# Kernel optimization log

Measured on AMD Instinct MI355X. Metric: run time of the kernel, lower is better.

## Reference

```python
import jax, jax.numpy as jnp
from jax import lax
import numpy as np

N, C, H, W = 8, 256, 96, 96
K = 5            # d_conv=4 forced odd -> 5 in FauxScan1D
HID = 2 * C      # ff_mult * dim


def setup_inputs() -> dict:
    key = jax.random.key(0)
    ks = iter(jax.random.split(key, 40))
    nrm = lambda *s: jax.random.normal(next(ks), s, jnp.float32) * 0.02
    inp = {'x': jax.random.normal(next(ks), (N, C, H, W), jnp.float32)}
    inp['ln1_w'] = jnp.ones((C,), jnp.float32)
    inp['ln1_b'] = jnp.zeros((C,), jnp.float32)
    inp['dw_w'] = nrm(3, 3, 1, C)   # depthwise 3x3, HWIO with feature_group_count=C
    inp['dw_b'] = jnp.zeros((C,), jnp.float32)
    for d in ('lr', 'rl', 'tb', 'bt'):
        inp[d + '_dw_w'] = nrm(K, 1, C)   # depthwise conv1d, WIO
        inp[d + '_dw_b'] = jnp.zeros((C,), jnp.float32)
        inp[d + '_g_w'] = nrm(C, C)       # 1x1 gate conv (out, in)
        inp[d + '_g_b'] = jnp.zeros((C,), jnp.float32)
    inp['fuse_w'] = nrm(C, C)
    inp['fuse_b'] = jnp.zeros((C,), jnp.float32)
    inp['ln2_w'] = jnp.ones((C,), jnp.float32)
    inp['ln2_b'] = jnp.zeros((C,), jnp.float32)
    inp['ff1_w'] = nrm(2 * HID, C)
    inp['ff1_b'] = jnp.zeros((2 * HID,), jnp.float32)
    inp['ff2_w'] = nrm(C, HID)
    inp['ff2_b'] = jnp.zeros((C,), jnp.float32)
    return inp


def _ln2d(x, w, b, eps=1e-6):
    # LayerNorm2d: per-(sample, channel) stats over H,W
    m = x.mean(axis=(2, 3), keepdims=True)
    v = ((x - m) ** 2).mean(axis=(2, 3), keepdims=True)
    return (x - m) * lax.rsqrt(v + eps) * w[None, :, None, None] + b[None, :, None, None]


def _scan1d(seq, dw_w, dw_b, g_w, g_b):
    # FauxScan1D: seq (B, L, C) -> dwconv1d(k=5, pad=2) * sigmoid(pointwise gate)
    c = seq.shape[-1]
    y = lax.conv_general_dilated(seq, dw_w, (1,), [(K // 2, K // 2)],
                                 dimension_numbers=('NWC', 'WIO', 'NWC'),
                                 feature_group_count=c) + dw_b
    g = jax.nn.sigmoid(jnp.einsum('blc,dc->bld', seq, g_w) + g_b)
    return y * g


def _forward(x, ln1_w, ln1_b, dw_w, dw_b,
             lr_dw_w, lr_dw_b, lr_g_w, lr_g_b,
             rl_dw_w, rl_dw_b, rl_g_w, rl_g_b,
             tb_dw_w, tb_dw_b, tb_g_w, tb_g_b,
             bt_dw_w, bt_dw_b, bt_g_w, bt_g_b,
             fuse_w, fuse_b, ln2_w, ln2_b, ff1_w, ff1_b, ff2_w, ff2_b):
    n, c, hh, ww = x.shape
    y = _ln2d(x, ln1_w, ln1_b)
    y = lax.conv_general_dilated(y, dw_w, (1, 1), [(1, 1), (1, 1)],
                                 dimension_numbers=('NCHW', 'HWIO', 'NCHW'),
                                 feature_group_count=c) + dw_b[None, :, None, None]
    y = jnp.transpose(y, (0, 2, 3, 1))  # NHWC
    # lr: rows as sequences
    o = _scan1d(y.reshape(n * hh, ww, c), lr_dw_w, lr_dw_b, lr_g_w, lr_g_b).reshape(n, hh, ww, c)
    # rl: flip width, scan, flip back
    yf = jnp.flip(y, 2).reshape(n * hh, ww, c)
    o = o + jnp.flip(_scan1d(yf, rl_dw_w, rl_dw_b, rl_g_w, rl_g_b).reshape(n, hh, ww, c), 2)
    # tb: columns as sequences
    yt = jnp.transpose(y, (0, 2, 1, 3)).reshape(n * ww, hh, c)
    o = o + jnp.transpose(_scan1d(yt, tb_dw_w, tb_dw_b, tb_g_w, tb_g_b).reshape(n, ww, hh, c), (0, 2, 1, 3))
    # bt: flip height, columns, scan, undo
    yb = jnp.transpose(jnp.flip(y, 1), (0, 2, 1, 3)).reshape(n * ww, hh, c)
    o = o + jnp.flip(jnp.transpose(_scan1d(yb, bt_dw_w, bt_dw_b, bt_g_w, bt_g_b).reshape(n, ww, hh, c), (0, 2, 1, 3)), 1)
    y = jnp.transpose(o, (0, 3, 1, 2))  # back to NCHW
    y = jnp.einsum('nchw,dc->ndhw', y, fuse_w) + fuse_b[None, :, None, None]
    x = x + y
    z = _ln2d(x, ln2_w, ln2_b)
    z = jnp.einsum('nchw,dc->ndhw', z, ff1_w) + ff1_b[None, :, None, None]
    a, g = jnp.split(z, 2, axis=1)  # GLU on channel dim
    z = a * jax.nn.sigmoid(g)
    z = jnp.einsum('nchw,dc->ndhw', z, ff2_w) + ff2_b[None, :, None, None]
    return x + z


def reference(x, ln1_w, ln1_b, dw_w, dw_b,
              lr_dw_w, lr_dw_b, lr_g_w, lr_g_b,
              rl_dw_w, rl_dw_b, rl_g_w, rl_g_b,
              tb_dw_w, tb_dw_b, tb_g_w, tb_g_b,
              bt_dw_w, bt_dw_b, bt_g_w, bt_g_b,
              fuse_w, fuse_b, ln2_w, ln2_b, ff1_w, ff1_b, ff2_w, ff2_b):
    return _forward(x, ln1_w, ln1_b, dw_w, dw_b,
                    lr_dw_w, lr_dw_b, lr_g_w, lr_g_b,
                    rl_dw_w, rl_dw_b, rl_g_w, rl_g_b,
                    tb_dw_w, tb_dw_b, tb_g_w, tb_g_b,
                    bt_dw_w, bt_dw_b, bt_g_w, bt_g_b,
                    fuse_w, fuse_b, ln2_w, ln2_b, ff1_w, ff1_b, ff2_w, ff2_b)
```

## Files before the change

kernel.cpp:

```cpp
#include <hip/hip_runtime.h>

#define TPB 256
#define HWSZ 9216

typedef __attribute__((ext_vector_type(8))) short short8x;
typedef __attribute__((ext_vector_type(4))) float f32x4;
typedef unsigned short ushort_t;
typedef unsigned int uint_t;

__device__ __forceinline__ float sigf(float v) { return 1.0f / (1.0f + __expf(-v)); }

__device__ __forceinline__ ushort_t f2bf(float f) {
  __bf16 h = (__bf16)f;
  return __builtin_bit_cast(ushort_t, h);
}
__device__ __forceinline__ float bf2f(ushort_t h) {
  return __uint_as_float(((uint_t)h) << 16);
}

__global__ __launch_bounds__(TPB) void k_pack(
    const float* __restrict__ lrg, const float* __restrict__ rlg,
    const float* __restrict__ tbg, const float* __restrict__ btg,
    const float* __restrict__ fusew, const float* __restrict__ ff1w,
    const float* __restrict__ ff2w,
    ushort_t* __restrict__ Gp, ushort_t* __restrict__ Ftp,
    ushort_t* __restrict__ W1p, ushort_t* __restrict__ W2p) {
  int i = blockIdx.x * TPB + threadIdx.x;
  if (i < 262144) {
    int d = i >> 16, r = i & 65535;
    int kt = r >> 13, nt = (r >> 9) & 15, l = (r >> 3) & 63, j = r & 7;
    int k = kt * 32 + (l >> 4) * 8 + j;
    int n_ = nt * 16 + (l & 15);
    const float* g = (d == 0) ? lrg : (d == 1) ? rlg : (d == 2) ? tbg : btg;
    Gp[i] = f2bf(g[n_ * 256 + k]);
  } else if (i < 327680) {
    int r = i - 262144;
    int kt = r >> 13, nt = (r >> 9) & 15, l = (r >> 3) & 63, j = r & 7;
    int k = kt * 32 + (l >> 4) * 8 + j;
    int n_ = nt * 16 + (l & 15);
    Ftp[r] = f2bf(fusew[n_ * 256 + k]);
  } else if (i < 589824) {
    int r = i - 327680;
    int kt = r >> 15, pb = (r >> 10) & 31, ag = (r >> 9) & 1;
    int l = (r >> 3) & 63, j = r & 7;
    int k = kt * 32 + (l >> 4) * 8 + j;
    int colb = pb * 16 + (l & 15);
    int col = ag ? (512 + colb) : colb;
    W1p[r] = f2bf(ff1w[col * 256 + k]);
  } else if (i < 720896) {
    int r = i - 589824;
    int kt = r >> 13, nt = (r >> 9) & 15, l = (r >> 3) & 63, j = r & 7;
    int k = kt * 32 + (l >> 4) * 8 + j;
    int n_ = nt * 16 + (l & 15);
    W2p[r] = f2bf(ff2w[n_ * 512 + k]);
  }
}

__global__ __launch_bounds__(TPB) void k_stats(const float* __restrict__ src,
                                               float* __restrict__ mean,
                                               float* __restrict__ rstd) {
  int nc = blockIdx.x;
  const float4* p = (const float4*)(src + (long)nc * HWSZ);
  float s = 0.f, s2 = 0.f;
  for (int i = threadIdx.x; i < 2304; i += TPB) {
    float4 v = p[i];
    s += (v.x + v.y) + (v.z + v.w);
    s2 = fmaf(v.x, v.x, fmaf(v.y, v.y, fmaf(v.z, v.z, fmaf(v.w, v.w, s2))));
  }
#pragma unroll
  for (int off = 32; off > 0; off >>= 1) {
    s += __shfl_down(s, off);
    s2 += __shfl_down(s2, off);
  }
  __shared__ float ls[4], ls2[4];
  int lane = threadIdx.x & 63, wv = threadIdx.x >> 6;
  if (lane == 0) { ls[wv] = s; ls2[wv] = s2; }
  __syncthreads();
  if (threadIdx.x == 0) {
    float S = ls[0] + ls[1] + ls[2] + ls[3];
    float S2 = ls2[0] + ls2[1] + ls2[2] + ls2[3];
    float m = S * (1.0f / HWSZ);
    float var = S2 * (1.0f / HWSZ) - m * m;
    mean[nc] = m;
    rstd[nc] = rsqrtf(fmaxf(var, 0.f) + 1e-6f);
  }
}

__global__ __launch_bounds__(TPB) void k_lndw(
    const float* __restrict__ x, const float* __restrict__ mean1,
    const float* __restrict__ rstd1, const float* __restrict__ ln1w,
    const float* __restrict__ ln1b, const float* __restrict__ dww,
    const float* __restrict__ dwb, ushort_t* __restrict__ y,
    ushort_t* __restrict__ yT) {
  __shared__ __align__(16) ushort_t xs[6 * 32 * 104];
  __shared__ __align__(16) ushort_t ot[2 * 96 * 32];
  __shared__ float sc[32], sh[32];

  int tid = threadIdx.x;
  int bid = blockIdx.x;
  int cb = (bid & 7) * 32;
  int hb = (bid >> 3) % 24;
  int n  = bid / 192;
  int h0 = hb * 4;

  if (tid < 32) {
    int c = cb + tid;
    int nc = n * 256 + c;
    float scale = rstd1[nc] * ln1w[c];
    sc[tid] = scale;
    sh[tid] = ln1b[c] - mean1[nc] * scale;
  }
  if (tid < 192) {
    xs[tid * 104 + 3] = 0;
    xs[tid * 104 + 100] = 0;
  }
  __syncthreads();

  for (int i = tid; i < 4608; i += TPB) {
    int rc = i / 24;
    int f4 = i - rc * 24;
    int row = rc >> 5, c = rc & 31;
    int hh = h0 - 1 + row;
    uint2 pk = make_uint2(0, 0);
    if (hh >= 0 && hh < 96) {
      float4 v = *(const float4*)(x + (long)(n * 256 + cb + c) * HWSZ +
                                  hh * 96 + f4 * 4);
      float scale = sc[c], shift = sh[c];
      ushort_t p0 = f2bf(fmaf(v.x, scale, shift));
      ushort_t p1 = f2bf(fmaf(v.y, scale, shift));
      ushort_t p2 = f2bf(fmaf(v.z, scale, shift));
      ushort_t p3 = f2bf(fmaf(v.w, scale, shift));
      pk.x = (uint_t)p0 | ((uint_t)p1 << 16);
      pk.y = (uint_t)p2 | ((uint_t)p3 << 16);
    }
    *(uint2*)(xs + rc * 104 + 4 + f4 * 4) = pk;
  }
  __syncthreads();

  int c = tid & 31, grp = tid >> 5;
  int w0 = grp * 12;
  float wgt[9];
#pragma unroll
  for (int t = 0; t < 9; ++t) wgt[t] = dww[t * 256 + cb + c];
  float bias = dwb[cb + c];

#pragma unroll
  for (int half = 0; half < 2; ++half) {
    float vals[2][12];
#pragma unroll
    for (int sub = 0; sub < 2; ++sub) {
      int orow = half * 2 + sub;
      float R[3][14];
#pragma unroll
      for (int rr = 0; rr < 3; ++rr) {
        const ushort_t* p = xs + ((orow + rr) * 32 + c) * 104;
        R[rr][0] = bf2f(p[3 + w0]);
        ushort4 q0 = *(const ushort4*)(p + 4 + w0);
        ushort4 q1 = *(const ushort4*)(p + 8 + w0);
        ushort4 q2 = *(const ushort4*)(p + 12 + w0);
        R[rr][1] = bf2f(q0.x);  R[rr][2] = bf2f(q0.y);
        R[rr][3] = bf2f(q0.z);  R[rr][4] = bf2f(q0.w);
        R[rr][5] = bf2f(q1.x);  R[rr][6] = bf2f(q1.y);
        R[rr][7] = bf2f(q1.z);  R[rr][8] = bf2f(q1.w);
        R[rr][9] = bf2f(q2.x);  R[rr][10] = bf2f(q2.y);
        R[rr][11] = bf2f(q2.z); R[rr][12] = bf2f(q2.w);
        R[rr][13] = bf2f(p[16 + w0]);
      }
#pragma unroll
      for (int k = 0; k < 12; ++k) {
        float acc = bias;
#pragma unroll
        for (int rr = 0; rr < 3; ++rr) {
          acc = fmaf(R[rr][k], wgt[rr * 3 + 0], acc);
          acc = fmaf(R[rr][k + 1], wgt[rr * 3 + 1], acc);
          acc = fmaf(R[rr][k + 2], wgt[rr * 3 + 2], acc);
        }
        vals[sub][k] = acc;
      }
    }
    if (half == 1) __syncthreads();
#pragma unroll
    for (int sub = 0; sub < 2; ++sub)
#pragma unroll
      for (int k = 0; k < 12; ++k)
        ot[(sub * 96 + w0 + k) * 32 + c] = f2bf(vals[sub][k]);
    __syncthreads();
#pragma unroll
    for (int it = 0; it < 3; ++it) {
      int u = it * 256 + tid;
      int r2 = (u >= 384) ? 1 : 0;
      int rem = u - r2 * 384;
      int w = rem >> 2, cq = rem & 3;
      uint4 v = *(const uint4*)(ot + (r2 * 96 + w) * 32 + cq * 8);
      int h = h0 + half * 2 + r2;
      *(uint4*)(y + ((long)(n * 96 + h) * 96 + w) * 256 + cb + cq * 8) = v;
      *(uint4*)(yT + ((long)(n * 96 + w) * 96 + h) * 256 + cb + cq * 8) = v;
    }
  }
}

__global__ __launch_bounds__(512, 4) void k_scan(
    const ushort_t* __restrict__ src, const uint4* __restrict__ gp4,
    const float* __restrict__ dwaw, const float* __restrict__ dwab,
    const float* __restrict__ gab, const float* __restrict__ dwbw,
    const float* __restrict__ dwbb, const float* __restrict__ gbb,
    ushort_t* __restrict__ dst) {
  __shared__ __align__(16) char pool[34816];
  char* ylds = pool;
  char* olds = pool + 26624;

  int tid = threadIdx.x;
  int bid = blockIdx.x;
  int seg = bid & 1, line = (bid >> 1) % 96, n = bid / 192;
  int p0 = seg * 48;
  long lbase = (long)(n * 96 + line) * 96;

  for (int u = tid; u < 52 * 32; u += 512) {
    int r = u >> 5, ks = u & 31;
    int q = p0 - 2 + r;
    uint4 v = make_uint4(0, 0, 0, 0);
    if (q >= 0 && q < 96)
      v = *(const uint4*)(src + (lbase + q) * 256 + ks * 8);
    *(uint4*)(ylds + r * 512 + ((ks * 16) ^ ((r & 7) << 4))) = v;
  }
  __syncthreads();

  int l = tid & 63, w = tid >> 6;
  int llo = l & 15, lhi = l >> 4;

  float part[3][2][4];

#pragma unroll
  for (int diri = 0; diri < 2; ++diri) {
    f32x4 acc[3][2];
#pragma unroll
    for (int mf = 0; mf < 3; ++mf)
#pragma unroll
      for (int ntl = 0; ntl < 2; ++ntl) acc[mf][ntl] = (f32x4){0.f, 0.f, 0.f, 0.f};

    const uint4* gbase = gp4 + ((long)(diri * 8) * 16 + w * 2) * 64 + l;
    short8x bc0 = *(const short8x*)(gbase);
    short8x bc1 = *(const short8x*)(gbase + 64);
#pragma unroll
    for (int kt = 0; kt < 8; ++kt) {
      short8x bn0, bn1;
      if (kt < 7) {
        bn0 = *(const short8x*)(gbase + (kt + 1) * 1024);
        bn1 = *(const short8x*)(gbase + (kt + 1) * 1024 + 64);
      }
      short8x a[3];
#pragma unroll
      for (int mf = 0; mf < 3; ++mf) {
        int arow = 2 + mf * 16 + llo;
        a[mf] = *(const short8x*)(ylds + arow * 512 +
                                  ((kt * 64 + lhi * 16) ^ ((arow & 7) << 4)));
      }
#pragma unroll
      for (int mf = 0; mf < 3; ++mf) {
        acc[mf][0] = __builtin_amdgcn_mfma_f32_16x16x32_bf16(a[mf], bc0, acc[mf][0], 0, 0, 0);
        acc[mf][1] = __builtin_amdgcn_mfma_f32_16x16x32_bf16(a[mf], bc1, acc[mf][1], 0, 0, 0);
      }
      bc0 = bn0;
      bc1 = bn1;
    }

    const float* dwv = diri ? dwbw : dwaw;
    const float* dbv = diri ? dwbb : dwab;
    const float* gbv = diri ? gbb : gab;
#pragma unroll
    for (int ntl = 0; ntl < 2; ++ntl) {
      int c = (w * 2 + ntl) * 16 + llo;
      float wt[5];
#pragma unroll
      for (int t = 0; t < 5; ++t)
        wt[t] = diri ? dwv[(4 - t) * 256 + c] : dwv[t * 256 + c];
      float cb = dbv[c], gb = gbv[c];
#pragma unroll
      for (int mf = 0; mf < 3; ++mf) {
        int pbase = mf * 16 + lhi * 4;
        float yv[8];
#pragma unroll
        for (int t = 0; t < 8; ++t) {
          int ry = pbase + t;
          yv[t] = bf2f(*(const ushort_t*)(ylds + ry * 512 +
                                          ((c * 2) ^ ((ry & 7) << 4))));
        }
#pragma unroll
        for (int r = 0; r < 4; ++r) {
          float conv = cb;
#pragma unroll
          for (int t = 0; t < 5; ++t) conv = fmaf(yv[r + t], wt[t], conv);
          float val = conv * sigf(acc[mf][ntl][r] + gb);
          if (diri == 0) part[mf][ntl][r] = val;
          else           part[mf][ntl][r] += val;
        }
      }
    }
  }

#pragma unroll
  for (int mf = 0; mf < 3; ++mf) {
    __syncthreads();
#pragma unroll
    for (int ntl = 0; ntl < 2; ++ntl) {
      int c = (w * 2 + ntl) * 16 + llo;
#pragma unroll
      for (int r = 0; r < 4; ++r) {
        int p = lhi * 4 + r;
        *(ushort_t*)(olds + p * 512 + ((c * 2) ^ ((p & 7) << 4))) =
            f2bf(part[mf][ntl][r]);
      }
    }
    __syncthreads();
    {
      int p = tid >> 5, ks = tid & 31;
      uint4 v = *(const uint4*)(olds + p * 512 + ((ks * 16) ^ ((p & 7) << 4)));
      *(uint4*)(dst + (lbase + p0 + mf * 16 + p) * 256 + ks * 8) = v;
    }
  }
}

__global__ __launch_bounds__(512, 4) void k_fuse(
    const ushort_t* __restrict__ o, const ushort_t* __restrict__ oT,
    const ushort_t* __restrict__ Ftp, const float* __restrict__ fuseb,
    const float* __restrict__ x, float* __restrict__ out) {
  __shared__ __align__(16) char pool[24576];

  int tid = threadIdx.x;
  int pix0 = blockIdx.x * 48;
  int n = pix0 / HWSZ, hw0 = pix0 % HWSZ;
  int h = hw0 / 96, w0 = hw0 % 96;

  for (int u = tid; u < 48 * 32; u += 512) {
    int r = u >> 5, ks = u & 31;
    uint4 va = *(const uint4*)(o + (long)(pix0 + r) * 256 + ks * 8);
    uint4 vb = *(const uint4*)(oT + ((long)(n * 96 + w0 + r) * 96 + h) * 256 + ks * 8);
    ushort_t* a8 = (ushort_t*)&va;
    ushort_t* b8 = (ushort_t*)&vb;
#pragma unroll
    for (int j = 0; j < 8; ++j) a8[j] = f2bf(bf2f(a8[j]) + bf2f(b8[j]));
    *(uint4*)(pool + r * 512 + ((ks * 16) ^ ((r & 7) << 4))) = va;
  }
  __syncthreads();

  int l = tid & 63, w = tid >> 6;
  int llo = l & 15, lhi = l >> 4;

  const uint4* fp4 = (const uint4*)Ftp;
  f32x4 acc[3][2];
#pragma unroll
  for (int mf = 0; mf < 3; ++mf)
#pragma unroll
    for (int ntl = 0; ntl < 2; ++ntl) acc[mf][ntl] = (f32x4){0.f, 0.f, 0.f, 0.f};

  const uint4* fbase = fp4 + (long)(w * 2) * 64 + l;
  short8x bc0 = *(const short8x*)(fbase);
  short8x bc1 = *(const short8x*)(fbase + 64);
#pragma unroll
  for (int kt = 0; kt < 8; ++kt) {
    short8x bn0, bn1;
    if (kt < 7) {
      bn0 = *(const short8x*)(fbase + (kt + 1) * 1024);
      bn1 = *(const short8x*)(fbase + (kt + 1) * 1024 + 64);
    }
    short8x a[3];
#pragma unroll
    for (int mf = 0; mf < 3; ++mf) {
      int arow = mf * 16 + llo;
      a[mf] = *(const short8x*)(pool + arow * 512 +
                                ((kt * 64 + lhi * 16) ^ ((arow & 7) << 4)));
    }
#pragma unroll
    for (int mf = 0; mf < 3; ++mf) {
      acc[mf][0] = __builtin_amdgcn_mfma_f32_16x16x32_bf16(a[mf], bc0, acc[mf][0], 0, 0, 0);
      acc[mf][1] = __builtin_amdgcn_mfma_f32_16x16x32_bf16(a[mf], bc1, acc[mf][1], 0, 0, 0);
    }
    bc0 = bn0;
    bc1 = bn1;
  }

#pragma unroll
  for (int mf = 0; mf < 3; ++mf)
#pragma unroll
    for (int ntl = 0; ntl < 2; ++ntl) {
      int c = (w * 2 + ntl) * 16 + llo;
      float fb = fuseb[c];
      long addr = (long)(n * 256 + c) * HWSZ + hw0 + mf * 16 + lhi * 4;
      float4 xv = *(const float4*)(x + addr);
      float4 ov;
      ov.x = xv.x + acc[mf][ntl][0] + fb;
      ov.y = xv.y + acc[mf][ntl][1] + fb;
      ov.z = xv.z + acc[mf][ntl][2] + fb;
      ov.w = xv.w + acc[mf][ntl][3] + fb;
      *(float4*)(out + addr) = ov;
    }
}

__global__ __launch_bounds__(512, 4) void k_ff1(
    const float* __restrict__ xres, const float* __restrict__ mean2,
    const float* __restrict__ rstd2, const float* __restrict__ ln2w,
    const float* __restrict__ ln2b, const ushort_t* __restrict__ W1p,
    const float* __restrict__ ff1b, ushort_t* __restrict__ u) {
  __shared__ char hA[96 * 512];
  __shared__ float sc[256], sh[256];

  int tid = threadIdx.x;
  int pix0 = blockIdx.x * 96;
  int n = pix0 / HWSZ, hw0 = pix0 % HWSZ;

  if (tid < 256) {
    int nc = n * 256 + tid;
    float scale = rstd2[nc] * ln2w[tid];
    sc[tid] = scale;
    sh[tid] = ln2b[tid] - mean2[nc] * scale;
  }
  __syncthreads();

  for (int i = tid; i < 6144; i += 512) {
    int cp = i / 48, pp = i % 48;
    int c0 = cp * 2;
    long base0 = (long)(n * 256 + c0) * HWSZ + hw0 + pp * 2;
    float2 v0 = *(const float2*)(xres + base0);
    float2 v1 = *(const float2*)(xres + base0 + HWSZ);
    float s0 = sc[c0], h0 = sh[c0];
    float s1 = sc[c0 + 1], h1 = sh[c0 + 1];
    int p0 = pp * 2;
    uint_t w0 = (uint_t)f2bf(fmaf(v0.x, s0, h0)) |
                ((uint_t)f2bf(fmaf(v1.x, s1, h1)) << 16);
    uint_t w1 = (uint_t)f2bf(fmaf(v0.y, s0, h0)) |
                ((uint_t)f2bf(fmaf(v1.y, s1, h1)) << 16);
    *(uint_t*)(hA + p0 * 512 + ((c0 * 2) ^ ((p0 & 7) << 4))) = w0;
    *(uint_t*)(hA + (p0 + 1) * 512 + ((c0 * 2) ^ (((p0 + 1) & 7) << 4))) = w1;
  }
  __syncthreads();

  int l = tid & 63, w = tid >> 6;
  int llo = l & 15, lhi = l >> 4;

  const uint4* W1p4 = (const uint4*)W1p;
#pragma unroll
  for (int q = 0; q < 4; ++q) {
    int pb = q * 8 + w;
    f32x4 ca[6][2];
#pragma unroll
    for (int mf = 0; mf < 6; ++mf) {
      ca[mf][0] = (f32x4){0.f, 0.f, 0.f, 0.f};
      ca[mf][1] = (f32x4){0.f, 0.f, 0.f, 0.f};
    }
    const uint4* wb = W1p4 + (long)(pb * 2) * 64 + l;
    short8x bca = *(const short8x*)(wb);
    short8x bcg = *(const short8x*)(wb + 64);
#pragma unroll
    for (int kt = 0; kt < 8; ++kt) {
      short8x bna, bng;
      if (kt < 7) {
        bna = *(const short8x*)(wb + (kt + 1) * 4096);
        bng = *(const short8x*)(wb + (kt + 1) * 4096 + 64);
      }
      short8x a[6];
#pragma unroll
      for (int mf = 0; mf < 6; ++mf) {
        int arow = mf * 16 + llo;
        a[mf] = *(const short8x*)(hA + arow * 512 +
                                  ((kt * 64 + lhi * 16) ^ ((arow & 7) << 4)));
      }
#pragma unroll
      for (int mf = 0; mf < 6; ++mf) {
        ca[mf][0] = __builtin_amdgcn_mfma_f32_16x16x32_bf16(a[mf], bca, ca[mf][0], 0, 0, 0);
        ca[mf][1] = __builtin_amdgcn_mfma_f32_16x16x32_bf16(a[mf], bcg, ca[mf][1], 0, 0, 0);
      }
      bca = bna;
      bcg = bng;
    }
    int ucol = pb * 16 + llo;
    float ba = ff1b[ucol], bg = ff1b[512 + ucol];
    int rb0 = (pix0 >> 2) + lhi;
#pragma unroll
    for (int mf = 0; mf < 6; ++mf) {
      ushort_t b0 = f2bf((ca[mf][0][0] + ba) * sigf(ca[mf][1][0] + bg));
      ushort_t b1 = f2bf((ca[mf][0][1] + ba) * sigf(ca[mf][1][1] + bg));
      ushort_t b2 = f2bf((ca[mf][0][2] + ba) * sigf(ca[mf][1][2] + bg));
      ushort_t b3 = f2bf((ca[mf][0][3] + ba) * sigf(ca[mf][1][3] + bg));
      uint2 pk;
      pk.x = (uint_t)b0 | ((uint_t)b1 << 16);
      pk.y = (uint_t)b2 | ((uint_t)b3 << 16);
      *(uint2*)(u + ((long)(rb0 + mf * 4) * 512 + ucol) * 4) = pk;
    }
  }
}

__global__ __launch_bounds__(512, 4) void k_ff2(
    const ushort_t* __restrict__ u, const ushort_t* __restrict__ W2p,
    const float* __restrict__ ff2b, float* __restrict__ out) {
  __shared__ __align__(16) char pool[24576];

  int tid = threadIdx.x;
  int pix0 = blockIdx.x * 96;
  int n = pix0 / HWSZ, hw0 = pix0 % HWSZ;
  int rb0 = pix0 >> 2;

  int l = tid & 63, w = tid >> 6;
  int llo = l & 15, lhi = l >> 4;

  const uint4* W2p4 = (const uint4*)W2p;

  uint2 st[6];
#pragma unroll
  for (int t = 0; t < 6; ++t) {
    int i = t * 512 + tid;
    int col = i & 127, rbl = i >> 7;
    st[t] = *(const uint2*)(u + ((long)(rb0 + rbl) * 512 + col) * 4);
  }

  f32x4 zacc[6][2];
#pragma unroll
  for (int mf = 0; mf < 6; ++mf) {
    zacc[mf][0] = (f32x4){0.f, 0.f, 0.f, 0.f};
    zacc[mf][1] = (f32x4){0.f, 0.f, 0.f, 0.f};
  }

#pragma unroll
  for (int kc = 0; kc < 4; ++kc) {
    if (kc) __syncthreads();
#pragma unroll
    for (int t = 0; t < 6; ++t) {
      int i = t * 512 + tid;
      int col = i & 127, rbl = i >> 7;
      int p = rbl * 4;
      ushort_t* b = (ushort_t*)&st[t];
#pragma unroll
      for (int k = 0; k < 4; ++k)
        *(ushort_t*)(pool + (p + k) * 256 + ((col * 2) ^ (((p + k) & 7) << 4))) = b[k];
    }
    __syncthreads();
    if (kc < 3) {
#pragma unroll
      for (int t = 0; t < 6; ++t) {
        int i = t * 512 + tid;
        int col = i & 127, rbl = i >> 7;
        st[t] = *(const uint2*)(u + ((long)(rb0 + rbl) * 512 + (kc + 1) * 128 + col) * 4);
      }
    }
#pragma unroll
    for (int ks = 0; ks < 4; ++ks) {
      int kt = kc * 4 + ks;
      short8x a[6];
#pragma unroll
      for (int mf = 0; mf < 6; ++mf) {
        int arow = mf * 16 + llo;
        a[mf] = *(const short8x*)(pool + arow * 256 +
                                  ((ks * 64 + lhi * 16) ^ ((arow & 7) << 4)));
      }
      short8x b0 = *(const short8x*)(W2p4 + (long)(kt * 16 + w * 2) * 64 + l);
      short8x b1 = *(const short8x*)(W2p4 + (long)(kt * 16 + w * 2 + 1) * 64 + l);
#pragma unroll
      for (int mf = 0; mf < 6; ++mf) {
        zacc[mf][0] = __builtin_amdgcn_mfma_f32_16x16x32_bf16(a[mf], b0, zacc[mf][0], 0, 0, 0);
        zacc[mf][1] = __builtin_amdgcn_mfma_f32_16x16x32_bf16(a[mf], b1, zacc[mf][1], 0, 0, 0);
      }
    }
  }

#pragma unroll
  for (int mf = 0; mf < 6; ++mf)
#pragma unroll
    for (int ntl = 0; ntl < 2; ++ntl) {
      int c = (w * 2 + ntl) * 16 + llo;
      float fb = ff2b[c];
      long addr = (long)(n * 256 + c) * HWSZ + hw0 + mf * 16 + lhi * 4;
      float4 ov = *(const float4*)(out + addr);
      ov.x += zacc[mf][ntl][0] + fb;
      ov.y += zacc[mf][ntl][1] + fb;
      ov.z += zacc[mf][ntl][2] + fb;
      ov.w += zacc[mf][ntl][3] + fb;
      *(float4*)(out + addr) = ov;
    }
}

extern "C" void kernel_launch(void* const* d_in, const int* in_sizes, int n_in,
                              void* d_out, int out_size, void* d_ws, size_t ws_size,
                              hipStream_t stream) {
  (void)in_sizes; (void)n_in; (void)out_size; (void)ws_size;
  const float* x     = (const float*)d_in[0];
  const float* ln1w  = (const float*)d_in[1];
  const float* ln1b  = (const float*)d_in[2];
  const float* dww   = (const float*)d_in[3];
  const float* dwb   = (const float*)d_in[4];
  const float* lr_w  = (const float*)d_in[5];
  const float* lr_b  = (const float*)d_in[6];
  const float* lr_gw = (const float*)d_in[7];
  const float* lr_gb = (const float*)d_in[8];
  const float* rl_w  = (const float*)d_in[9];
  const float* rl_b  = (const float*)d_in[10];
  const float* rl_gw = (const float*)d_in[11];
  const float* rl_gb = (const float*)d_in[12];
  const float* tb_w  = (const float*)d_in[13];
  const float* tb_b  = (const float*)d_in[14];
  const float* tb_gw = (const float*)d_in[15];
  const float* tb_gb = (const float*)d_in[16];
  const float* bt_w  = (const float*)d_in[17];
  const float* bt_b  = (const float*)d_in[18];
  const float* bt_gw = (const float*)d_in[19];
  const float* bt_gb = (const float*)d_in[20];
  const float* fusew = (const float*)d_in[21];
  const float* fuseb = (const float*)d_in[22];
  const float* ln2w  = (const float*)d_in[23];
  const float* ln2b  = (const float*)d_in[24];
  const float* ff1w  = (const float*)d_in[25];
  const float* ff1b  = (const float*)d_in[26];
  const float* ff2w  = (const float*)d_in[27];
  const float* ff2b  = (const float*)d_in[28];

  float* out = (float*)d_out;
  ushort_t* y  = (ushort_t*)d_ws;
  ushort_t* yT = y + 18874368;
  ushort_t* o  = yT + 18874368;
  ushort_t* oT = o + 18874368;
  ushort_t* uu = y;
  float* mean1 = (float*)(oT + 18874368);
  float* rstd1 = mean1 + 2048;
  float* mean2 = rstd1 + 2048;
  float* rstd2 = mean2 + 2048;
  ushort_t* Gp  = (ushort_t*)(rstd2 + 2048);
  ushort_t* Ftp = Gp + 262144;
  ushort_t* W1p = Ftp + 65536;
  ushort_t* W2p = W1p + 262144;

  k_pack<<<2816, TPB, 0, stream>>>(lr_gw, rl_gw, tb_gw, bt_gw, fusew, ff1w, ff2w,
                                   Gp, Ftp, W1p, W2p);
  k_stats<<<2048, TPB, 0, stream>>>(x, mean1, rstd1);
  k_lndw<<<1536, TPB, 0, stream>>>(x, mean1, rstd1, ln1w, ln1b, dww, dwb, y, yT);
  k_scan<<<1536, 512, 0, stream>>>(y, (const uint4*)Gp,
                                   lr_w, lr_b, lr_gb, rl_w, rl_b, rl_gb, o);
  k_scan<<<1536, 512, 0, stream>>>(yT, (const uint4*)(Gp + 131072),
                                   tb_w, tb_b, tb_gb, bt_w, bt_b, bt_gb, oT);
  k_fuse<<<1536, 512, 0, stream>>>(o, oT, Ftp, fuseb, x, out);
  k_stats<<<2048, TPB, 0, stream>>>(out, mean2, rstd2);
  k_ff1<<<768, 512, 0, stream>>>(out, mean2, rstd2, ln2w, ln2b, W1p, ff1b, uu);
  k_ff2<<<768, 512, 0, stream>>>(uu, W2p, ff2b, out);
}
```

Before: 314.2 us.

## Fuse LN2 statistics into fuse kernel via atomics; pad LDS rows instead of swizzle

The fuse epilogue now accumulates per-(sample, channel) sum and sum of squares, reduces them with wave shuffles and adds them into global buffers with atomics. This removes the separate k_stats pass that re-read the full fp32 residual tensor. k_ff1 then derives mean and rstd from E[x^2]-E[x]^2, which costs some numerical robustness. Separately, the XOR-swizzled LDS layouts in the scan, fuse, ff1 and ff2 kernels are replaced with padded row strides (528 and 272 bytes), which simplifies address math but raises shared memory use.

```diff
diff --git a/kernel.cpp b/kernel.cpp
--- a/kernel.cpp
+++ b/kernel.cpp
@@ -2,6 +2,8 @@
 
 #define TPB 256
 #define HWSZ 9216
+#define RS 528
+#define RS2 272
 
 typedef __attribute__((ext_vector_type(8))) short short8x;
 typedef __attribute__((ext_vector_type(4))) float f32x4;
@@ -205,9 +207,9 @@
     const float* __restrict__ gab, const float* __restrict__ dwbw,
     const float* __restrict__ dwbb, const float* __restrict__ gbb,
     ushort_t* __restrict__ dst) {
-  __shared__ __align__(16) char pool[34816];
+  __shared__ __align__(16) char pool[52 * RS + 16 * RS];
   char* ylds = pool;
-  char* olds = pool + 26624;
+  char* olds = pool + 52 * RS;
 
   int tid = threadIdx.x;
   int bid = blockIdx.x;
@@ -221,7 +223,7 @@
     uint4 v = make_uint4(0, 0, 0, 0);
     if (q >= 0 && q < 96)
       v = *(const uint4*)(src + (lbase + q) * 256 + ks * 8);
-    *(uint4*)(ylds + r * 512 + ((ks * 16) ^ ((r & 7) << 4))) = v;
+    *(uint4*)(ylds + r * RS + ks * 16) = v;
   }
   __syncthreads();
 
@@ -252,8 +254,7 @@
 #pragma unroll
       for (int mf = 0; mf < 3; ++mf) {
         int arow = 2 + mf * 16 + llo;
-        a[mf] = *(const short8x*)(ylds + arow * 512 +
-                                  ((kt * 64 + lhi * 16) ^ ((arow & 7) << 4)));
+        a[mf] = *(const short8x*)(ylds + arow * RS + kt * 64 + lhi * 16);
       }
 #pragma unroll
       for (int mf = 0; mf < 3; ++mf) {
@@ -282,8 +283,7 @@
 #pragma unroll
         for (int t = 0; t < 8; ++t) {
           int ry = pbase + t;
-          yv[t] = bf2f(*(const ushort_t*)(ylds + ry * 512 +
-                                          ((c * 2) ^ ((ry & 7) << 4))));
+          yv[t] = bf2f(*(const ushort_t*)(ylds + ry * RS + c * 2));
         }
 #pragma unroll
         for (int r = 0; r < 4; ++r) {
@@ -307,14 +307,13 @@
 #pragma unroll
       for (int r = 0; r < 4; ++r) {
         int p = lhi * 4 + r;
-        *(ushort_t*)(olds + p * 512 + ((c * 2) ^ ((p & 7) << 4))) =
-            f2bf(part[mf][ntl][r]);
+        *(ushort_t*)(olds + p * RS + c * 2) = f2bf(part[mf][ntl][r]);
       }
     }
     __syncthreads();
     {
       int p = tid >> 5, ks = tid & 31;
-      uint4 v = *(const uint4*)(olds + p * 512 + ((ks * 16) ^ ((p & 7) << 4)));
+      uint4 v = *(const uint4*)(olds + p * RS + ks * 16);
       *(uint4*)(dst + (lbase + p0 + mf * 16 + p) * 256 + ks * 8) = v;
     }
   }
@@ -323,8 +322,9 @@
 __global__ __launch_bounds__(512, 4) void k_fuse(
     const ushort_t* __restrict__ o, const ushort_t* __restrict__ oT,
     const ushort_t* __restrict__ Ftp, const float* __restrict__ fuseb,
-    const float* __restrict__ x, float* __restrict__ out) {
-  __shared__ __align__(16) char pool[24576];
+    const float* __restrict__ x, float* __restrict__ out,
+    float* __restrict__ sumb, float* __restrict__ sqb) {
+  __shared__ __align__(16) char pool[48 * RS];
 
   int tid = threadIdx.x;
   int pix0 = blockIdx.x * 48;
@@ -339,7 +339,7 @@
     ushort_t* b8 = (ushort_t*)&vb;
 #pragma unroll
     for (int j = 0; j < 8; ++j) a8[j] = f2bf(bf2f(a8[j]) + bf2f(b8[j]));
-    *(uint4*)(pool + r * 512 + ((ks * 16) ^ ((r & 7) << 4))) = va;
+    *(uint4*)(pool + r * RS + ks * 16) = va;
   }
   __syncthreads();
 
@@ -367,8 +367,7 @@
 #pragma unroll
     for (int mf = 0; mf < 3; ++mf) {
       int arow = mf * 16 + llo;
-      a[mf] = *(const short8x*)(pool + arow * 512 +
-                                ((kt * 64 + lhi * 16) ^ ((arow & 7) << 4)));
+      a[mf] = *(const short8x*)(pool + arow * RS + kt * 64 + lhi * 16);
     }
 #pragma unroll
     for (int mf = 0; mf < 3; ++mf) {
@@ -379,6 +378,7 @@
     bc1 = bn1;
   }
 
+  float s1[2] = {0.f, 0.f}, s2[2] = {0.f, 0.f};
 #pragma unroll
   for (int mf = 0; mf < 3; ++mf)
 #pragma unroll
@@ -393,15 +393,32 @@
       ov.z = xv.z + acc[mf][ntl][2] + fb;
       ov.w = xv.w + acc[mf][ntl][3] + fb;
       *(float4*)(out + addr) = ov;
-    }
+      s1[ntl] += (ov.x + ov.y) + (ov.z + ov.w);
+      s2[ntl] += fmaf(ov.x, ov.x, fmaf(ov.y, ov.y, fmaf(ov.z, ov.z, ov.w * ov.w)));
+    }
+#pragma unroll
+  for (int ntl = 0; ntl < 2; ++ntl) {
+    s1[ntl] += __shfl_xor(s1[ntl], 16);
+    s2[ntl] += __shfl_xor(s2[ntl], 16);
+    s1[ntl] += __shfl_xor(s1[ntl], 32);
+    s2[ntl] += __shfl_xor(s2[ntl], 32);
+  }
+  if (lhi == 0) {
+#pragma unroll
+    for (int ntl = 0; ntl < 2; ++ntl) {
+      int c = (w * 2 + ntl) * 16 + llo;
+      atomicAdd(&sumb[n * 256 + c], s1[ntl]);
+      atomicAdd(&sqb[n * 256 + c], s2[ntl]);
+    }
+  }
 }
 
 __global__ __launch_bounds__(512, 4) void k_ff1(
-    const float* __restrict__ xres, const float* __restrict__ mean2,
-    const float* __restrict__ rstd2, const float* __restrict__ ln2w,
+    const float* __restrict__ xres, const float* __restrict__ sumb,
+    const float* __restrict__ sqb, const float* __restrict__ ln2w,
     const float* __restrict__ ln2b, const ushort_t* __restrict__ W1p,
     const float* __restrict__ ff1b, ushort_t* __restrict__ u) {
-  __shared__ char hA[96 * 512];
+  __shared__ __align__(16) char hA[96 * RS];
   __shared__ float sc[256], sh[256];
 
   int tid = threadIdx.x;
@@ -410,9 +427,12 @@
 
   if (tid < 256) {
     int nc = n * 256 + tid;
-    float scale = rstd2[nc] * ln2w[tid];
+    float m = sumb[nc] * (1.0f / HWSZ);
+    float var = sqb[nc] * (1.0f / HWSZ) - m * m;
+    float rstd = rsqrtf(fmaxf(var, 0.f) + 1e-6f);
+    float scale = rstd * ln2w[tid];
     sc[tid] = scale;
-    sh[tid] = ln2b[tid] - mean2[nc] * scale;
+    sh[tid] = ln2b[tid] - m * scale;
   }
   __syncthreads();
 
@@ -429,8 +449,8 @@
                 ((uint_t)f2bf(fmaf(v1.x, s1, h1)) << 16);
     uint_t w1 = (uint_t)f2bf(fmaf(v0.y, s0, h0)) |
                 ((uint_t)f2bf(fmaf(v1.y, s1, h1)) << 16);
-    *(uint_t*)(hA + p0 * 512 + ((c0 * 2) ^ ((p0 & 7) << 4))) = w0;
-    *(uint_t*)(hA + (p0 + 1) * 512 + ((c0 * 2) ^ (((p0 + 1) & 7) << 4))) = w1;
+    *(uint_t*)(hA + p0 * RS + c0 * 2) = w0;
+    *(uint_t*)(hA + (p0 + 1) * RS + c0 * 2) = w1;
   }
   __syncthreads();
 
@@ -461,8 +481,7 @@
 #pragma unroll
       for (int mf = 0; mf < 6; ++mf) {
         int arow = mf * 16 + llo;
-        a[mf] = *(const short8x*)(hA + arow * 512 +
-                                  ((kt * 64 + lhi * 16) ^ ((arow & 7) << 4)));
+        a[mf] = *(const short8x*)(hA + arow * RS + kt * 64 + lhi * 16);
       }
 #pragma unroll
       for (int mf = 0; mf < 6; ++mf) {
@@ -492,7 +511,7 @@
 __global__ __launch_bounds__(512, 4) void k_ff2(
     const ushort_t* __restrict__ u, const ushort_t* __restrict__ W2p,
     const float* __restrict__ ff2b, float* __restrict__ out) {
-  __shared__ __align__(16) char pool[24576];
+  __shared__ __align__(16) char pool[96 * RS2];
 
   int tid = threadIdx.x;
   int pix0 = blockIdx.x * 96;
@@ -530,7 +549,7 @@
       ushort_t* b = (ushort_t*)&st[t];
 #pragma unroll
       for (int k = 0; k < 4; ++k)
-        *(ushort_t*)(pool + (p + k) * 256 + ((col * 2) ^ (((p + k) & 7) << 4))) = b[k];
+        *(ushort_t*)(pool + (p + k) * RS2 + col * 2) = b[k];
     }
     __syncthreads();
     if (kc < 3) {
@@ -548,8 +567,7 @@
 #pragma unroll
       for (int mf = 0; mf < 6; ++mf) {
         int arow = mf * 16 + llo;
-        a[mf] = *(const short8x*)(pool + arow * 256 +
-                                  ((ks * 64 + lhi * 16) ^ ((arow & 7) << 4)));
+        a[mf] = *(const short8x*)(pool + arow * RS2 + ks * 64 + lhi * 16);
       }
       short8x b0 = *(const short8x*)(W2p4 + (long)(kt * 16 + w * 2) * 64 + l);
       short8x b1 = *(const short8x*)(W2p4 + (long)(kt * 16 + w * 2 + 1) * 64 + l);
@@ -619,13 +637,14 @@
   ushort_t* uu = y;
   float* mean1 = (float*)(oT + 18874368);
   float* rstd1 = mean1 + 2048;
-  float* mean2 = rstd1 + 2048;
-  float* rstd2 = mean2 + 2048;
-  ushort_t* Gp  = (ushort_t*)(rstd2 + 2048);
+  float* sumb  = rstd1 + 2048;
+  float* sqb   = sumb + 2048;
+  ushort_t* Gp  = (ushort_t*)(sqb + 2048);
   ushort_t* Ftp = Gp + 262144;
   ushort_t* W1p = Ftp + 65536;
   ushort_t* W2p = W1p + 262144;
 
+  hipMemsetAsync(sumb, 0, 4096 * sizeof(float), stream);
   k_pack<<<2816, TPB, 0, stream>>>(lr_gw, rl_gw, tb_gw, bt_gw, fusew, ff1w, ff2w,
                                    Gp, Ftp, W1p, W2p);
   k_stats<<<2048, TPB, 0, stream>>>(x, mean1, rstd1);
@@ -634,8 +653,7 @@
                                    lr_w, lr_b, lr_gb, rl_w, rl_b, rl_gb, o);
   k_scan<<<1536, 512, 0, stream>>>(yT, (const uint4*)(Gp + 131072),
                                    tb_w, tb_b, tb_gb, bt_w, bt_b, bt_gb, oT);
-  k_fuse<<<1536, 512, 0, stream>>>(o, oT, Ftp, fuseb, x, out);
-  k_stats<<<2048, TPB, 0, stream>>>(out, mean2, rstd2);
-  k_ff1<<<768, 512, 0, stream>>>(out, mean2, rstd2, ln2w, ln2b, W1p, ff1b, uu);
+  k_fuse<<<1536, 512, 0, stream>>>(o, oT, Ftp, fuseb, x, out, sumb, sqb);
+  k_ff1<<<768, 512, 0, stream>>>(out, sumb, sqb, ln2w, ln2b, W1p, ff1b, uu);
   k_ff2<<<768, 512, 0, stream>>>(uu, W2p, ff2b, out);
 }
```

After: 316.8 us. Within noise of the previous version (+0.8%).
